# Kernel tuning notes

Measured on AMD Instinct MI355X. Metric: run time of the kernel, lower is better.

Reference implementation:

```python
import jax, jax.numpy as jnp
import numpy as np

N_NODES = 16384
N_EDGES = 32768
D = 128          # node feature / hidden dim
EDGE_DIM = 10    # bond featurizer one-hot dim
EH = 32          # edge_hidden_dim in the NNConv MLPs


def _nnconv(x, src, dst, edge_attr, l1w, l1b, l2w, l2b, root, bias):
    """PyG NNConv with aggr='mean': out_i = x_i @ root + mean_{e: dst=i} x_{src_e} @ W(e) + bias."""
    E = edge_attr.shape[0]
    h = jax.nn.relu(edge_attr @ l1w + l1b)              # [E, EH]
    W = (h @ l2w + l2b).reshape(E, D, D)                # per-edge weight matrices [E, D, D]
    msg = jnp.einsum('ei,eio->eo', x[src], W)           # gather + per-edge matmul [E, D]
    s = jax.ops.segment_sum(msg, dst, num_segments=N_NODES)
    cnt = jax.ops.segment_sum(jnp.ones((E, 1), x.dtype), dst, num_segments=N_NODES)
    agg = s / jnp.maximum(cnt, 1.0)                     # scatter-mean (0 for isolated nodes)
    return x @ root + agg + bias


def setup_inputs() -> dict:
    key = jax.random.key(0)
    ks = jax.random.split(key, 14)
    x = jax.random.normal(ks[0], (N_NODES, D), dtype=jnp.float32)
    edge_index = jax.random.randint(ks[1], (2, N_EDGES), 0, N_NODES, dtype=jnp.int64)
    edge_attr = jax.random.uniform(ks[2], (N_EDGES, EDGE_DIM), dtype=jnp.float32)

    def lin(k, fan_in, fan_out):
        return jax.random.normal(k, (fan_in, fan_out), dtype=jnp.float32) / np.sqrt(fan_in)

    return {
        'x': x, 'edge_index': edge_index, 'edge_attr': edge_attr,
        # subgraph_conv1 (128 -> 128)
        'w1_l1': lin(ks[3], EDGE_DIM, EH), 'b1_l1': jnp.zeros((EH,), jnp.float32),
        'w1_l2': lin(ks[4], EH, D * D),    'b1_l2': jnp.zeros((D * D,), jnp.float32),
        'w1_root': lin(ks[5], D, D),       'b1': jnp.zeros((D,), jnp.float32),
        # subgraph_conv2 (128 -> 128), applied twice with shared weights
        'w2_l1': lin(ks[6], EDGE_DIM, EH), 'b2_l1': jnp.zeros((EH,), jnp.float32),
        'w2_l2': lin(ks[7], EH, D * D),    'b2_l2': jnp.zeros((D * D,), jnp.float32),
        'w2_root': lin(ks[8], D, D),       'b2': jnp.zeros((D,), jnp.float32),
    }


def reference(x, edge_index, edge_attr,
              w1_l1, b1_l1, w1_l2, b1_l2, w1_root, b1,
              w2_l1, b2_l1, w2_l2, b2_l2, w2_root, b2):
    src, dst = edge_index[0], edge_index[1]
    h = jax.nn.relu(_nnconv(x, src, dst, edge_attr, w1_l1, b1_l1, w1_l2, b1_l2, w1_root, b1))
    h = jax.nn.relu(_nnconv(h, src, dst, edge_attr, w2_l1, b2_l1, w2_l2, b2_l2, w2_root, b2))
    h = _nnconv(h, src, dst, edge_attr, w2_l1, b2_l1, w2_l2, b2_l2, w2_root, b2)
    return h
```

## Files before the change

### kernel.cpp

```cpp
#include <hip/hip_runtime.h>

#define N_NODES 16384
#define N_EDGES 32768
#define D 128
#define EDGE_DIM 10
#define KH 32
#define BM 128
#define XMS 136
#define XST 136
#define NBL 32

typedef _Float16 f16;
typedef _Float16 f16x4 __attribute__((ext_vector_type(4)));
typedef _Float16 f16x8 __attribute__((ext_vector_type(8)));
typedef float f32x4 __attribute__((ext_vector_type(4)));

__global__ __launch_bounds__(256) void deg_pack_kernel(
    const int* __restrict__ ei, int* __restrict__ deg,
    const float* __restrict__ w1l2, const float* __restrict__ w2l2,
    const float* __restrict__ b1l2, const float* __restrict__ b2l2,
    const float* __restrict__ rt1, const float* __restrict__ rt2,
    f16* __restrict__ Bp1, f16* __restrict__ Bp2,
    f16* __restrict__ Rp1, f16* __restrict__ Rp2) {
  int y = blockIdx.y;
  if (y == 0) {
    int e = blockIdx.x * 256 + threadIdx.x;
    if (e < N_EDGES) atomicAdd(&deg[ei[N_EDGES + e]], 1);
    return;
  }
  if (blockIdx.x >= D * D / 256) return;
  int t = blockIdx.x * 256 + threadIdx.x;
  int j = y - 1;
  if (j < 2) {
    const float* l2w = j ? w2l2 : w1l2;
    f16* Bp = j ? Bp2 : Bp1;
    f16 tmp[KH];
#pragma unroll
    for (int k = 0; k < KH; k++) tmp[k] = (f16)l2w[(size_t)k * (D * D) + t];
    f16x8* dst = (f16x8*)(Bp + (size_t)t * KH);
#pragma unroll
    for (int c = 0; c < 4; c++) dst[c] = *(f16x8*)&tmp[c * 8];
  } else {
    const float* src = (j == 2) ? b1l2 : (j == 3) ? b2l2 : (j == 4) ? rt1 : rt2;
    f16* dst = (j == 2) ? (Bp1 + (size_t)D * D * KH)
             : (j == 3) ? (Bp2 + (size_t)D * D * KH)
             : (j == 4) ? Rp1 : Rp2;
    int i = t >> 7, o = t & 127;
    dst[((size_t)(i >> 5) * D + o) * KH + (i & 31)] = (f16)src[t];
  }
}

__global__ __launch_bounds__(1024) void scan_kernel(
    const int* __restrict__ deg, int* __restrict__ rs, int* __restrict__ fill) {
  __shared__ int part[1024];
  int t = threadIdx.x;
  int base = t * 16;
  int loc[16], s = 0;
#pragma unroll
  for (int j = 0; j < 16; j++) { loc[j] = deg[base + j]; s += loc[j]; }
  part[t] = s;
  __syncthreads();
  for (int off = 1; off < 1024; off <<= 1) {
    int add = (t >= off) ? part[t - off] : 0;
    __syncthreads();
    part[t] += add;
    __syncthreads();
  }
  int run = t ? part[t - 1] : 0;
#pragma unroll
  for (int j = 0; j < 16; j++) {
    rs[base + j] = run; fill[base + j] = run; run += loc[j];
  }
  if (t == 1023) rs[N_NODES] = run;
}

__global__ __launch_bounds__(256) void scatter_kernel(
    const int* __restrict__ ei, int* __restrict__ fill,
    int* __restrict__ perm, int* __restrict__ srcs) {
  int e = blockIdx.x * blockDim.x + threadIdx.x;
  if (e < N_EDGES) {
    int pos = atomicAdd(&fill[ei[N_EDGES + e]], 1);
    perm[pos] = e;
    srcs[pos] = ei[e];
  }
}

__global__ __launch_bounds__(256) void edge_mlp_kernel(
    const float* __restrict__ ea, const int* __restrict__ perm,
    const float* __restrict__ w1l1, const float* __restrict__ b1l1,
    const float* __restrict__ w2l1, const float* __restrict__ b2l1,
    f16* __restrict__ h1, f16* __restrict__ h2) {
  int p = blockIdx.x * blockDim.x + threadIdx.x;
  const float* l1w = blockIdx.y ? w2l1 : w1l1;
  const float* l1b = blockIdx.y ? b2l1 : b1l1;
  f16* h = blockIdx.y ? h2 : h1;
  int e = perm[p];
  float a[EDGE_DIM];
#pragma unroll
  for (int d = 0; d < EDGE_DIM; d++) a[d] = ea[e * EDGE_DIM + d];
  f16 hv[KH];
#pragma unroll
  for (int k = 0; k < KH; k++) {
    float acc = l1b[k];
#pragma unroll
    for (int d = 0; d < EDGE_DIM; d++) acc += a[d] * l1w[d * KH + k];
    hv[k] = (f16)fmaxf(acc, 0.0f);
  }
  f16x8* dst = (f16x8*)(h + (size_t)p * KH);
#pragma unroll
  for (int c = 0; c < 4; c++) dst[c] = *(f16x8*)&hv[c * 8];
}

__global__ __launch_bounds__(512, 2) void msg_mfma_kernel(
    const float* __restrict__ xin, const f16* __restrict__ hf,
    const f16* __restrict__ Bp, const int* __restrict__ srcs,
    f16* __restrict__ msgf) {
  __shared__ f16 Xs[BM][XMS];
  __shared__ f16 Hs[BM][KH];
  int t = threadIdx.x;
  int e0 = blockIdx.x * BM;

  ((f16x8*)Hs)[t] = ((const f16x8*)(hf + (size_t)e0 * KH))[t];
  {
    int r = t >> 2, q = t & 3;
    int s = srcs[e0 + r];
    const float4* src = (const float4*)(xin + (size_t)s * D + q * 32);
    f16* dst = &Xs[r][q * 32];
#pragma unroll
    for (int c = 0; c < 8; c++) {
      float4 v = src[c];
      f16x4 h4 = {(f16)v.x, (f16)v.y, (f16)v.z, (f16)v.w};
      *(f16x4*)(dst + c * 4) = h4;
    }
  }

  int L = t & 63, w = t >> 6;
  int quad = L >> 4, lm = L & 15;
  int n0 = w * 16;

  const f16* bl = Bp + ((size_t)(n0 + lm)) * KH + quad * 8;
  const size_t istr = (size_t)D * KH;

  f32x4 acc[8];
#pragma unroll
  for (int mt = 0; mt < 8; mt++)
    acc[mt] = (f32x4){0.f, 0.f, 0.f, 0.f};

  f16x8 bufA[4], bufB[4];

  auto loadg = [&](f16x8 (&buf)[4], int basei) {
#pragma unroll
    for (int jj = 0; jj < 4; jj++)
      buf[jj] = *(const f16x8*)(bl + (size_t)(basei + jj) * istr);
  };

  f16x8 hreg[8];

  auto compute = [&](f16x8 (&buf)[4], int ig) {
    f16x4 xv[8];
#pragma unroll
    for (int mt = 0; mt < 8; mt++)
      xv[mt] = *(const f16x4*)&Xs[mt * 16 + lm][ig];
#pragma unroll
    for (int jj = 0; jj < 4; jj++) {
#pragma unroll
      for (int mt = 0; mt < 8; mt++) {
        f16 xs = xv[mt][jj];
        f16x8 xb = {xs, xs, xs, xs, xs, xs, xs, xs};
        f16x8 a = hreg[mt] * xb;
        acc[mt] = __builtin_amdgcn_mfma_f32_16x16x32_f16(a, buf[jj], acc[mt], 0, 0, 0);
      }
    }
  };

  loadg(bufA, 0);
  __syncthreads();

#pragma unroll
  for (int mt = 0; mt < 8; mt++)
    hreg[mt] = *(const f16x8*)&Hs[mt * 16 + lm][quad * 8];

#pragma unroll 1
  for (int g = 0; g < 16; g++) {
    loadg(bufB, 8 * g + 4);
    compute(bufA, 8 * g);
    loadg(bufA, 8 * g + 8);
    compute(bufB, 8 * g + 4);
  }

  {
    const f16* bb = Bp + (size_t)D * D * KH;
#pragma unroll
    for (int g2 = 0; g2 < 4; g2++) {
      f16x8 b0 = *(const f16x8*)(bb + ((size_t)g2 * D + n0 + lm) * KH + quad * 8);
      int lc = g2 * 32 + quad * 8;
#pragma unroll
      for (int mt = 0; mt < 8; mt++) {
        f16x8 a = *(const f16x8*)&Xs[mt * 16 + lm][lc];
        acc[mt] = __builtin_amdgcn_mfma_f32_16x16x32_f16(a, b0, acc[mt], 0, 0, 0);
      }
    }
  }

#pragma unroll
  for (int mt = 0; mt < 8; mt++)
#pragma unroll
    for (int r = 0; r < 4; r++) {
      f16* mg = msgf + (size_t)(e0 + mt * 16 + quad * 4 + r) * D + n0 + lm;
      mg[0] = (f16)acc[mt][r];
    }
}

__global__ __launch_bounds__(256) void node_update_kernel(
    const float* __restrict__ xin, const f16* __restrict__ msg,
    const int* __restrict__ rs, const f16* __restrict__ Rp,
    const float* __restrict__ bias, float* __restrict__ out, int do_relu) {
  __shared__ f16 Xs[NBL][XST];
  __shared__ float Sls[NBL][D];
  int t = threadIdx.x;
  int nb = blockIdx.x * NBL;

  {
    int r = t >> 3, q = t & 7;
    const float4* src = (const float4*)(xin + (size_t)(nb + r) * D + q * 16);
    f16* dst = &Xs[r][q * 16];
#pragma unroll
    for (int c = 0; c < 4; c++) {
      float4 v = src[c];
      f16x4 h4 = {(f16)v.x, (f16)v.y, (f16)v.z, (f16)v.w};
      *(f16x4*)(dst + c * 4) = h4;
    }
  }
  __syncthreads();

  {
    int nl = t >> 3, o0 = (t & 7) * 16;
    int n = nb + nl;
    int a = rs[n], b = rs[n + 1];
    float sum[16];
#pragma unroll
    for (int j = 0; j < 16; j++) sum[j] = 0.f;
    for (int r = a; r < b; r++) {
      f16x8 a0 = *(const f16x8*)(msg + (size_t)r * D + o0);
      f16x8 a1 = *(const f16x8*)(msg + (size_t)r * D + o0 + 8);
#pragma unroll
      for (int j = 0; j < 8; j++) {
        sum[j]     += (float)a0[j];
        sum[8 + j] += (float)a1[j];
      }
    }
    float inv = 1.0f / (float)max(b - a, 1);
#pragma unroll
    for (int j = 0; j < 16; j++) Sls[nl][o0 + j] = sum[j] * inv;
  }
  __syncthreads();

  int L = t & 63, w = t >> 6;
  int quad = L >> 4, lm = L & 15;
  int n0 = w * 32;
  f32x4 acc[2][2];
#pragma unroll
  for (int mt = 0; mt < 2; mt++)
#pragma unroll
    for (int nt = 0; nt < 2; nt++)
      acc[mt][nt] = (f32x4){0.f, 0.f, 0.f, 0.f};
#pragma unroll
  for (int s4 = 0; s4 < 4; s4++) {
    const f16* b2l = Rp + ((size_t)s4 * D + n0 + lm) * KH + quad * 8;
    f16x8 b0 = *(const f16x8*)b2l;
    f16x8 b1 = *(const f16x8*)(b2l + 16 * KH);
#pragma unroll
    for (int mt = 0; mt < 2; mt++) {
      f16x8 a = *(const f16x8*)&Xs[mt * 16 + lm][s4 * 32 + quad * 8];
      acc[mt][0] = __builtin_amdgcn_mfma_f32_16x16x32_f16(a, b0, acc[mt][0], 0, 0, 0);
      acc[mt][1] = __builtin_amdgcn_mfma_f32_16x16x32_f16(a, b1, acc[mt][1], 0, 0, 0);
    }
  }
#pragma unroll
  for (int mt = 0; mt < 2; mt++)
#pragma unroll
    for (int r = 0; r < 4; r++) {
      Sls[mt * 16 + quad * 4 + r][n0 + lm] += acc[mt][0][r];
      Sls[mt * 16 + quad * 4 + r][n0 + 16 + lm] += acc[mt][1][r];
    }
  __syncthreads();

  {
    int o = t & 127, g = t >> 7;
    float bo = bias[o];
    for (int q = g * 16; q < g * 16 + 16; q++) {
      float v = bo + Sls[q][o];
      out[(size_t)(nb + q) * D + o] = do_relu ? fmaxf(v, 0.0f) : v;
    }
  }
}

extern "C" void kernel_launch(void* const* d_in, const int* in_sizes, int n_in,
                              void* d_out, int out_size, void* d_ws, size_t ws_size,
                              hipStream_t stream) {
  const float* x      = (const float*)d_in[0];
  const int*   ei     = (const int*)d_in[1];
  const float* ea     = (const float*)d_in[2];
  const float* w1_l1  = (const float*)d_in[3];
  const float* b1_l1  = (const float*)d_in[4];
  const float* w1_l2  = (const float*)d_in[5];
  const float* b1_l2  = (const float*)d_in[6];
  const float* w1_rt  = (const float*)d_in[7];
  const float* b1     = (const float*)d_in[8];
  const float* w2_l1  = (const float*)d_in[9];
  const float* b2_l1  = (const float*)d_in[10];
  const float* w2_l2  = (const float*)d_in[11];
  const float* b2_l2  = (const float*)d_in[12];
  const float* w2_rt  = (const float*)d_in[13];
  const float* b2     = (const float*)d_in[14];
  float* out = (float*)d_out;

  const size_t BPSZ = (size_t)D * D * KH + (size_t)D * D + 32768;
  f16* h1f = (f16*)d_ws;
  f16* h2f = h1f + (size_t)N_EDGES * KH;
  f16* Bp1 = h2f + (size_t)N_EDGES * KH;
  f16* Bp2 = Bp1 + BPSZ;
  f16* Rp1 = Bp2 + BPSZ;
  f16* Rp2 = Rp1 + (size_t)D * D;
  int* deg  = (int*)(Rp2 + (size_t)D * D);
  int* rs   = deg + N_NODES;
  int* fill = rs + N_NODES + 128;
  int* perm = fill + N_NODES;
  int* srcs = perm + N_EDGES;
  f16* msg  = (f16*)(srcs + N_EDGES);

  hipMemsetAsync(deg, 0, N_NODES * sizeof(int), stream);
  deg_pack_kernel<<<dim3(N_EDGES / 256, 7), 256, 0, stream>>>(
      ei, deg, w1_l2, w2_l2, b1_l2, b2_l2, w1_rt, w2_rt, Bp1, Bp2, Rp1, Rp2);
  scan_kernel<<<1, 1024, 0, stream>>>(deg, rs, fill);
  scatter_kernel<<<N_EDGES / 256, 256, 0, stream>>>(ei, fill, perm, srcs);
  edge_mlp_kernel<<<dim3(N_EDGES / 256, 2), 256, 0, stream>>>(
      ea, perm, w1_l1, b1_l1, w2_l1, b2_l1, h1f, h2f);

  msg_mfma_kernel<<<N_EDGES / BM, 512, 0, stream>>>(x, h1f, Bp1, srcs, msg);
  node_update_kernel<<<N_NODES / NBL, 256, 0, stream>>>(x, msg, rs, Rp1, b1, out, 1);
  msg_mfma_kernel<<<N_EDGES / BM, 512, 0, stream>>>(out, h2f, Bp2, srcs, msg);
  node_update_kernel<<<N_NODES / NBL, 256, 0, stream>>>(out, msg, rs, Rp2, b2, out, 1);
  msg_mfma_kernel<<<N_EDGES / BM, 512, 0, stream>>>(out, h2f, Bp2, srcs, msg);
  node_update_kernel<<<N_NODES / NBL, 256, 0, stream>>>(out, msg, rs, Rp2, b2, out, 0);
}
```

Measured before the change: 269.5 us.

## Retile per-edge message MFMA kernel to 2x4 edge-by-output tiles per wave

Changes the wave work split in the message kernel from 16 output columns across all 128 edges to 32 edges by 64 output columns per wave. Each wave now does fewer x-scaled A-operand builds (2 instead of 8 per k-step) but loads 4x more B fragments from global per step. Register pressure rises (16 buffered B vectors per buffer), so launch bounds drop to one block per CU. The intent is to cut redundant VALU A-construction work at the cost of more B traffic and lower occupancy.

```diff
diff --git a/kernel.cpp b/kernel.cpp
--- a/kernel.cpp
+++ b/kernel.cpp
@@ -111,7 +111,7 @@
   for (int c = 0; c < 4; c++) dst[c] = *(f16x8*)&hv[c * 8];
 }
 
-__global__ __launch_bounds__(512, 2) void msg_mfma_kernel(
+__global__ __launch_bounds__(512, 1) void msg_mfma_kernel(
     const float* __restrict__ xin, const f16* __restrict__ hf,
     const f16* __restrict__ Bp, const int* __restrict__ srcs,
     f16* __restrict__ msgf) {
@@ -136,39 +136,49 @@
 
   int L = t & 63, w = t >> 6;
   int quad = L >> 4, lm = L & 15;
-  int n0 = w * 16;
+  int eq = (w & 3) * 32;
+  int n0 = (w >> 2) * 64;
 
   const f16* bl = Bp + ((size_t)(n0 + lm)) * KH + quad * 8;
   const size_t istr = (size_t)D * KH;
-
-  f32x4 acc[8];
-#pragma unroll
-  for (int mt = 0; mt < 8; mt++)
-    acc[mt] = (f32x4){0.f, 0.f, 0.f, 0.f};
-
-  f16x8 bufA[4], bufB[4];
-
-  auto loadg = [&](f16x8 (&buf)[4], int basei) {
-#pragma unroll
-    for (int jj = 0; jj < 4; jj++)
-      buf[jj] = *(const f16x8*)(bl + (size_t)(basei + jj) * istr);
+  const size_t ntstr = (size_t)16 * KH;
+
+  f32x4 acc[2][4];
+#pragma unroll
+  for (int mt = 0; mt < 2; mt++)
+#pragma unroll
+    for (int nt = 0; nt < 4; nt++)
+      acc[mt][nt] = (f32x4){0.f, 0.f, 0.f, 0.f};
+
+  f16x8 bufA[4][4], bufB[4][4];
+
+  auto loadg = [&](f16x8 (&buf)[4][4], int basei) {
+#pragma unroll
+    for (int jj = 0; jj < 4; jj++) {
+      const f16* bi = bl + (size_t)(basei + jj) * istr;
+#pragma unroll
+      for (int nt = 0; nt < 4; nt++)
+        buf[jj][nt] = *(const f16x8*)(bi + nt * ntstr);
+    }
   };
 
-  f16x8 hreg[8];
-
-  auto compute = [&](f16x8 (&buf)[4], int ig) {
-    f16x4 xv[8];
-#pragma unroll
-    for (int mt = 0; mt < 8; mt++)
-      xv[mt] = *(const f16x4*)&Xs[mt * 16 + lm][ig];
+  f16x8 hreg[2];
+
+  auto compute = [&](f16x8 (&buf)[4][4], int ig) {
+    f16x4 xv[2];
+#pragma unroll
+    for (int mt = 0; mt < 2; mt++)
+      xv[mt] = *(const f16x4*)&Xs[eq + mt * 16 + lm][ig];
 #pragma unroll
     for (int jj = 0; jj < 4; jj++) {
 #pragma unroll
-      for (int mt = 0; mt < 8; mt++) {
+      for (int mt = 0; mt < 2; mt++) {
         f16 xs = xv[mt][jj];
         f16x8 xb = {xs, xs, xs, xs, xs, xs, xs, xs};
         f16x8 a = hreg[mt] * xb;
-        acc[mt] = __builtin_amdgcn_mfma_f32_16x16x32_f16(a, buf[jj], acc[mt], 0, 0, 0);
+#pragma unroll
+        for (int nt = 0; nt < 4; nt++)
+          acc[mt][nt] = __builtin_amdgcn_mfma_f32_16x16x32_f16(a, buf[jj][nt], acc[mt][nt], 0, 0, 0);
       }
     }
   };
@@ -177,8 +187,8 @@
   __syncthreads();
 
 #pragma unroll
-  for (int mt = 0; mt < 8; mt++)
-    hreg[mt] = *(const f16x8*)&Hs[mt * 16 + lm][quad * 8];
+  for (int mt = 0; mt < 2; mt++)
+    hreg[mt] = *(const f16x8*)&Hs[eq + mt * 16 + lm][quad * 8];
 
 #pragma unroll 1
   for (int g = 0; g < 16; g++) {
@@ -192,22 +202,29 @@
     const f16* bb = Bp + (size_t)D * D * KH;
 #pragma unroll
     for (int g2 = 0; g2 < 4; g2++) {
-      f16x8 b0 = *(const f16x8*)(bb + ((size_t)g2 * D + n0 + lm) * KH + quad * 8);
+      f16x8 b0[4];
+#pragma unroll
+      for (int nt = 0; nt < 4; nt++)
+        b0[nt] = *(const f16x8*)(bb + ((size_t)g2 * D + n0 + nt * 16 + lm) * KH + quad * 8);
       int lc = g2 * 32 + quad * 8;
 #pragma unroll
-      for (int mt = 0; mt < 8; mt++) {
-        f16x8 a = *(const f16x8*)&Xs[mt * 16 + lm][lc];
-        acc[mt] = __builtin_amdgcn_mfma_f32_16x16x32_f16(a, b0, acc[mt], 0, 0, 0);
+      for (int mt = 0; mt < 2; mt++) {
+        f16x8 a = *(const f16x8*)&Xs[eq + mt * 16 + lm][lc];
+#pragma unroll
+        for (int nt = 0; nt < 4; nt++)
+          acc[mt][nt] = __builtin_amdgcn_mfma_f32_16x16x32_f16(a, b0[nt], acc[mt][nt], 0, 0, 0);
       }
     }
   }
 
 #pragma unroll
-  for (int mt = 0; mt < 8; mt++)
+  for (int mt = 0; mt < 2; mt++)
 #pragma unroll
     for (int r = 0; r < 4; r++) {
-      f16* mg = msgf + (size_t)(e0 + mt * 16 + quad * 4 + r) * D + n0 + lm;
-      mg[0] = (f16)acc[mt][r];
+      f16* mg = msgf + (size_t)(e0 + eq + mt * 16 + quad * 4 + r) * D + n0 + lm;
+#pragma unroll
+      for (int nt = 0; nt < 4; nt++)
+        mg[nt * 16] = (f16)acc[mt][nt][r];
     }
 }
 
```

After: 340.4 us. 26.3% more time.
